# Performance work log

Measured on AMD Instinct MI355X. Metric: run time of the kernel, lower is better.

## Reference

```python
import jax, jax.numpy as jnp
import numpy as np

N_NODES = 50000
N_EDGES = 800000
IN_FEAT = 256
UNITS = 128
NEG_SLOPE = 0.2  # tf.nn.leaky_relu default alpha


def setup_inputs() -> dict:
    key = jax.random.key(0)
    k1, k2, k3, k4 = jax.random.split(key, 4)
    node_states = jax.random.normal(k1, (N_NODES, IN_FEAT), dtype=jnp.float32)
    edges = jax.random.randint(k2, (N_EDGES, 2), 0, N_NODES, dtype=jnp.int64)
    kernel = jax.random.normal(k3, (IN_FEAT, UNITS), dtype=jnp.float32) * 0.05
    kernel_attention = jax.random.normal(k4, (2 * UNITS, 1), dtype=jnp.float32) * 0.05
    return {"node_states": node_states, "edges": edges,
            "kernel": kernel, "kernel_attention": kernel_attention}


def reference(node_states, edges, kernel, kernel_attention):
    # node_states: [N, F], edges: [E, 2] (col 0 = target/segment, col 1 = source)
    n_nodes = node_states.shape[0]
    tgt = edges[:, 0]
    src = edges[:, 1]

    h = node_states @ kernel  # [N, U]

    # attention score per edge: leaky_relu(concat(h[tgt], h[src]) @ a)
    # split the attention vector so the two matmuls happen per-node (same math,
    # avoids materializing the [E, 2U] concat)
    u = h.shape[1]
    a_tgt = (h @ kernel_attention[:u]).squeeze(-1)  # [N]
    a_src = (h @ kernel_attention[u:]).squeeze(-1)  # [N]
    scores = jax.nn.leaky_relu(a_tgt[tgt] + a_src[src], NEG_SLOPE)  # [E]
    scores = jnp.exp(jnp.clip(scores, -2.0, 2.0))

    # segment softmax over edges grouped by target node
    denom = jax.ops.segment_sum(scores, tgt, num_segments=n_nodes)  # [N]
    attn = scores / denom[tgt]  # [E]

    # weighted aggregation of neighbor features
    out = jax.ops.segment_sum(h[src] * attn[:, None], tgt, num_segments=n_nodes)  # [N, U]
    return out
```

## Files before the change

kernel.cpp:

```cpp
#include <hip/hip_runtime.h>
#include <hip/hip_bf16.h>

#define N_NODES 50000
#define N_EDGES 800000
#define IN_FEAT 256
#define UNITS   128
#define BUCKET  64

typedef unsigned short ushort_t;
typedef __bf16 bf16x8 __attribute__((ext_vector_type(8)));
typedef float  f32x4  __attribute__((ext_vector_type(4)));
typedef unsigned short ushort8 __attribute__((ext_vector_type(8)));

__device__ __forceinline__ ushort_t bfbits(float f) {
    __bf16 b = (__bf16)f;
    return __builtin_bit_cast(ushort_t, b);
}

__device__ __forceinline__ void cvt8(const float4& f0, const float4& f1,
                                     ushort_t* dst) {
    bf16x8 u;
    u[0] = (__bf16)f0.x; u[1] = (__bf16)f0.y; u[2] = (__bf16)f0.z; u[3] = (__bf16)f0.w;
    u[4] = (__bf16)f1.x; u[5] = (__bf16)f1.y; u[6] = (__bf16)f1.z; u[7] = (__bf16)f1.w;
    *(bf16x8*)dst = u;
}

__global__ __launch_bounds__(256) void prep_wt_zero(const float* __restrict__ W,
                                                    ushort_t* __restrict__ Wt,
                                                    int* __restrict__ cnt, int M) {
    int i = blockIdx.x * 256 + threadIdx.x;
    if (i < UNITS * IN_FEAT) {
        int n = i >> 8;
        int k = i & 255;
        Wt[i] = bfbits(W[(size_t)k * UNITS + n]);
    }
    if (i < M) cnt[i] = 0;
}

__global__ __launch_bounds__(256) void gemm_mfma(const float* __restrict__ A,
                                                 const ushort_t* __restrict__ Wt,
                                                 const float* __restrict__ ka,
                                                 ushort_t* __restrict__ Hb,
                                                 float* __restrict__ a_tgt,
                                                 float* __restrict__ a_src, int M) {
    __shared__ __align__(16) ushort_t Bs[128 * 264];
    __shared__ __align__(16) ushort_t As[2 * 64 * 40];
    __shared__ float spt[64][2];
    __shared__ float sps[64][2];
    const int tid  = threadIdx.x;
    const int lane = tid & 63;
    const int wv   = tid >> 6;
    const int wy   = wv >> 1;
    const int wx   = wv & 1;
    const int row0 = blockIdx.x * 64;
    const int quad = lane >> 4;
    const int cl   = lane & 15;

    f32x4 acc[2][4] = {};

#pragma unroll
    for (int t = 0; t < 16; ++t) {
        int j = t * 256 + tid;
        int r = j >> 5;
        int c = (j & 31) * 8;
        *(ushort8*)(Bs + r * 264 + c) = *(const ushort8*)(Wt + r * 256 + c);
    }

    const int ar = tid >> 2, aq = tid & 3;
    const int gr = min(row0 + ar, M - 1);
    const float* aptr = A + (size_t)gr * IN_FEAT + aq * 8;
    ushort_t*    asw  = As + ar * 40 + aq * 8;

    {
        float4 f0 = *(const float4*)(aptr);
        float4 f1 = *(const float4*)(aptr + 4);
        cvt8(f0, f1, asw);
    }
    __syncthreads();

    for (int kc = 0; kc < IN_FEAT; kc += 32) {
        const int cur = (kc >> 5) & 1;
        const bool more = (kc + 32 < IN_FEAT);
        float4 g0, g1;
        if (more) {
            g0 = *(const float4*)(aptr + kc + 32);
            g1 = *(const float4*)(aptr + kc + 36);
        }

        bf16x8 af[2], bff[4];
        const ushort_t* asb = As + cur * 2560;
#pragma unroll
        for (int mi = 0; mi < 2; ++mi)
            af[mi] = *(const bf16x8*)(asb + (wy * 32 + mi * 16 + cl) * 40 + quad * 8);
#pragma unroll
        for (int ni = 0; ni < 4; ++ni)
            bff[ni] = *(const bf16x8*)(Bs + (wx * 64 + ni * 16 + cl) * 264 + kc + quad * 8);
#pragma unroll
        for (int mi = 0; mi < 2; ++mi)
#pragma unroll
            for (int ni = 0; ni < 4; ++ni)
                acc[mi][ni] = __builtin_amdgcn_mfma_f32_16x16x32_bf16(
                    af[mi], bff[ni], acc[mi][ni], 0, 0, 0);

        if (more)
            cvt8(g0, g1, As + (cur ^ 1) * 2560 + ar * 40 + aq * 8);
        __syncthreads();
    }

#pragma unroll
    for (int mi = 0; mi < 2; ++mi) {
#pragma unroll
        for (int ni = 0; ni < 4; ++ni) {
            int col = wx * 64 + ni * 16 + cl;
#pragma unroll
            for (int r = 0; r < 4; ++r) {
                int row = row0 + wy * 32 + mi * 16 + quad * 4 + r;
                if (row < M)
                    Hb[(size_t)row * UNITS + col] = bfbits(acc[mi][ni][r]);
            }
        }
    }

    float kt[4], ks[4];
#pragma unroll
    for (int ni = 0; ni < 4; ++ni) {
        int col = wx * 64 + ni * 16 + cl;
        kt[ni] = ka[col];
        ks[ni] = ka[UNITS + col];
    }
#pragma unroll
    for (int mi = 0; mi < 2; ++mi) {
        float pt[4] = {}, ps[4] = {};
#pragma unroll
        for (int ni = 0; ni < 4; ++ni)
#pragma unroll
            for (int r = 0; r < 4; ++r) {
                pt[r] += acc[mi][ni][r] * kt[ni];
                ps[r] += acc[mi][ni][r] * ks[ni];
            }
#pragma unroll
        for (int r = 0; r < 4; ++r) {
#pragma unroll
            for (int m = 1; m < 16; m <<= 1) {
                pt[r] += __shfl_xor(pt[r], m);
                ps[r] += __shfl_xor(ps[r], m);
            }
            if (cl == 0) {
                int rl = wy * 32 + mi * 16 + quad * 4 + r;
                spt[rl][wx] = pt[r];
                sps[rl][wx] = ps[r];
            }
        }
    }
    __syncthreads();
    if (tid < 64) {
        int row = row0 + tid;
        if (row < M) {
            a_tgt[row] = spt[tid][0] + spt[tid][1];
            a_src[row] = sps[tid][0] + sps[tid][1];
        }
    }
}

__device__ __forceinline__ float edge_score(float at, float as) {
    float s = at + as;
    s = s > 0.f ? s : 0.2f * s;
    s = fminf(fmaxf(s, -2.f), 2.f);
    return __expf(s);
}

__global__ __launch_bounds__(256) void scatter(const int* __restrict__ edges,
                                               const float* __restrict__ at,
                                               const float* __restrict__ as,
                                               int* __restrict__ cnt,
                                               int2* __restrict__ csr, int E) {
    int e = blockIdx.x * 256 + threadIdx.x;
    if (e >= E) return;
    int2 ts = ((const int2*)edges)[e];
    float sc = edge_score(at[ts.x], as[ts.y]);
    int r = atomicAdd(&cnt[ts.x], 1);
    if (r < BUCKET)
        csr[(size_t)ts.x * BUCKET + r] = make_int2(ts.y, __float_as_int(sc));
}

__global__ __launch_bounds__(256) void aggregate(const ushort_t* __restrict__ Hb,
                                                 const int* __restrict__ cnt,
                                                 const int2* __restrict__ csr,
                                                 float* __restrict__ out, int M) {
    int wid  = (int)((blockIdx.x * 256 + threadIdx.x) >> 6);
    int lane = threadIdx.x & 63;
    if (wid >= M) return;
    const int g = lane >> 4;
    const int c = lane & 15;
    const int deg = min(cnt[wid], BUCKET);

    int   s_v = 0;
    float w_v = 0.f;
    if (lane < deg) {
        int2 sw = csr[(size_t)wid * BUCKET + lane];
        s_v = sw.x;
        w_v = __int_as_float(sw.y);
    }

    float acc[8] = {};
    int nstep = (deg + 3) >> 2;
#pragma unroll 4
    for (int t = 0; t < nstep; ++t) {
        int slot = t * 4 + g;
        int   src = __shfl(s_v, slot);
        float w   = __shfl(w_v, slot);
        uint4 u = *(const uint4*)(Hb + (size_t)src * UNITS + c * 8);
        acc[0] += w * __uint_as_float(u.x << 16);
        acc[1] += w * __uint_as_float(u.x & 0xffff0000u);
        acc[2] += w * __uint_as_float(u.y << 16);
        acc[3] += w * __uint_as_float(u.y & 0xffff0000u);
        acc[4] += w * __uint_as_float(u.z << 16);
        acc[5] += w * __uint_as_float(u.z & 0xffff0000u);
        acc[6] += w * __uint_as_float(u.w << 16);
        acc[7] += w * __uint_as_float(u.w & 0xffff0000u);
    }

#pragma unroll
    for (int i = 0; i < 8; ++i) {
        acc[i] += __shfl_xor(acc[i], 16);
        acc[i] += __shfl_xor(acc[i], 32);
    }
    float wacc = w_v;
#pragma unroll
    for (int off = 32; off > 0; off >>= 1) wacc += __shfl_xor(wacc, off);
    float scale = (deg > 0) ? 1.0f / wacc : 0.0f;

    if (g == 0) {
        float4 o0 = make_float4(acc[0] * scale, acc[1] * scale,
                                acc[2] * scale, acc[3] * scale);
        float4 o1 = make_float4(acc[4] * scale, acc[5] * scale,
                                acc[6] * scale, acc[7] * scale);
        float* dst = out + (size_t)wid * UNITS + c * 8;
        *(float4*)dst       = o0;
        *(float4*)(dst + 4) = o1;
    }
}

extern "C" void kernel_launch(void* const* d_in, const int* in_sizes, int n_in,
                              void* d_out, int out_size, void* d_ws, size_t ws_size,
                              hipStream_t stream) {
    const float* node_states = (const float*)d_in[0];
    const int*   edges       = (const int*)d_in[1];
    const float* W           = (const float*)d_in[2];
    const float* ka          = (const float*)d_in[3];
    float*       out         = (float*)d_out;

    const int M = N_NODES, E = N_EDGES;

    ushort_t* hb     = (ushort_t*)d_ws;
    float*    a_tgt  = (float*)(hb + (size_t)M * UNITS);
    float*    a_src  = a_tgt + M;
    int*      cnt    = (int*)(a_src + M);
    int2*     csr    = (int2*)(cnt + M + 2);
    ushort_t* wt     = (ushort_t*)csr;

    prep_wt_zero<<<(M + 255) / 256, 256, 0, stream>>>(W, wt, cnt, M);
    gemm_mfma   <<<(M + 63) / 64, 256, 0, stream>>>(node_states, wt, ka, hb,
                                                    a_tgt, a_src, M);
    scatter     <<<(E + 255) / 256, 256, 0, stream>>>(edges, a_tgt, a_src,
                                                      cnt, csr, E);
    aggregate   <<<(M * 64 + 255) / 256, 256, 0, stream>>>(hb, cnt, csr, out, M);
}
```

Measured before the change: 185.2 us.

## Replace global-atomic edge scatter with two-pass binning by target range

Swaps the single scatter kernel, which did one global atomicAdd per edge on per-node counters, for two passes. The first bins edges into 196 target-node ranges using a shared-memory histogram, a block scan and staging. The second processes each bin in one 1024-thread block, counting with shared-memory atomics and writing the per-node counts directly, so the counter zeroing is no longer needed. This cuts contended global atomics and scattered writes, at the cost of an extra kernel launch, an extra pass over the edges, and only 196 blocks in the second pass. It also drops edges if a bin holds more than BIN_CAP entries.

Measured after the change: 167.7 us. -9.5%, faster.

```diff
diff --git a/kernel.cpp b/kernel.cpp
--- a/kernel.cpp
+++ b/kernel.cpp
@@ -6,6 +6,10 @@
 #define IN_FEAT 256
 #define UNITS   128
 #define BUCKET  64
+#define BIN_SHIFT 8
+#define NBINS   196
+#define BIN_CAP 4608
+#define CHUNK   4096
 
 typedef unsigned short ushort_t;
 typedef __bf16 bf16x8 __attribute__((ext_vector_type(8)));
@@ -27,14 +31,14 @@
 
 __global__ __launch_bounds__(256) void prep_wt_zero(const float* __restrict__ W,
                                                     ushort_t* __restrict__ Wt,
-                                                    int* __restrict__ cnt, int M) {
+                                                    int* __restrict__ gbin) {
     int i = blockIdx.x * 256 + threadIdx.x;
     if (i < UNITS * IN_FEAT) {
         int n = i >> 8;
         int k = i & 255;
         Wt[i] = bfbits(W[(size_t)k * UNITS + n]);
     }
-    if (i < M) cnt[i] = 0;
+    if (i < 256) gbin[i] = 0;
 }
 
 __global__ __launch_bounds__(256) void gemm_mfma(const float* __restrict__ A,
@@ -169,18 +173,105 @@
     return __expf(s);
 }
 
-__global__ __launch_bounds__(256) void scatter(const int* __restrict__ edges,
-                                               const float* __restrict__ at,
-                                               const float* __restrict__ as,
-                                               int* __restrict__ cnt,
-                                               int2* __restrict__ csr, int E) {
-    int e = blockIdx.x * 256 + threadIdx.x;
-    if (e >= E) return;
-    int2 ts = ((const int2*)edges)[e];
-    float sc = edge_score(at[ts.x], as[ts.y]);
-    int r = atomicAdd(&cnt[ts.x], 1);
-    if (r < BUCKET)
-        csr[(size_t)ts.x * BUCKET + r] = make_int2(ts.y, __float_as_int(sc));
+__global__ __launch_bounds__(256) void bin_edges(const int* __restrict__ edges,
+                                                 int* __restrict__ gbin,
+                                                 int2* __restrict__ binbuf, int E) {
+    __shared__ int  hist[256];
+    __shared__ int  sbase[256];
+    __shared__ int  runoff[256];
+    __shared__ int  gbase[256];
+    __shared__ int  wsum[4];
+    __shared__ int2 stage[CHUNK];
+    const int tid  = threadIdx.x;
+    const int lane = tid & 63, wv = tid >> 6;
+    const int e0   = blockIdx.x * CHUNK;
+
+    hist[tid] = 0;
+    __syncthreads();
+
+    int2 er[16];
+    int  eb[16];
+#pragma unroll
+    for (int j = 0; j < 16; ++j) {
+        int idx = e0 + j * 256 + tid;
+        if (idx < E) {
+            er[j] = ((const int2*)edges)[idx];
+            eb[j] = er[j].x >> BIN_SHIFT;
+            atomicAdd(&hist[eb[j]], 1);
+        } else eb[j] = -1;
+    }
+    __syncthreads();
+
+    int h = hist[tid];
+    int incl = h;
+#pragma unroll
+    for (int off = 1; off < 64; off <<= 1) {
+        int t = __shfl_up(incl, off);
+        if (lane >= off) incl += t;
+    }
+    if (lane == 63) wsum[wv] = incl;
+    __syncthreads();
+    int excl = incl - h;
+#pragma unroll
+    for (int w = 0; w < 4; ++w) if (w < wv) excl += wsum[w];
+    sbase[tid]  = excl;
+    runoff[tid] = excl;
+    __syncthreads();
+
+    if (h > 0) gbase[tid] = atomicAdd(&gbin[tid], h);
+
+#pragma unroll
+    for (int j = 0; j < 16; ++j) {
+        if (eb[j] >= 0) {
+            int p = atomicAdd(&runoff[eb[j]], 1);
+            stage[p] = er[j];
+        }
+    }
+    __syncthreads();
+
+    int total = sbase[255] + hist[255];
+    for (int p = tid; p < total; p += 256) {
+        int2 ts = stage[p];
+        int b   = ts.x >> BIN_SHIFT;
+        int dst = gbase[b] + (p - sbase[b]);
+        if (dst < BIN_CAP)
+            binbuf[(size_t)b * BIN_CAP + dst] = ts;
+    }
+}
+
+__global__ __launch_bounds__(1024) void bucket_scatter(const int2* __restrict__ binbuf,
+                                                       const int* __restrict__ gbin,
+                                                       const float* __restrict__ at,
+                                                       const float* __restrict__ as,
+                                                       int* __restrict__ cnt,
+                                                       int2* __restrict__ csr, int M) {
+    __shared__ int   lcnt[256];
+    __shared__ float atl[256];
+    const int tid = threadIdx.x;
+    const int bin = blockIdx.x;
+    const int t0  = bin << BIN_SHIFT;
+    if (tid < 256) {
+        lcnt[tid] = 0;
+        int t = t0 + tid;
+        atl[tid] = (t < M) ? at[t] : 0.f;
+    }
+    __syncthreads();
+
+    const int bcnt = min(gbin[bin], BIN_CAP);
+    const int2* src = binbuf + (size_t)bin * BIN_CAP;
+    for (int p = tid; p < bcnt; p += 1024) {
+        int2 ts = src[p];
+        int lt  = ts.x - t0;
+        float sc = edge_score(atl[lt], as[ts.y]);
+        int r = atomicAdd(&lcnt[lt], 1);
+        if (r < BUCKET)
+            csr[(size_t)ts.x * BUCKET + r] = make_int2(ts.y, __float_as_int(sc));
+    }
+    __syncthreads();
+    if (tid < 256) {
+        int t = t0 + tid;
+        if (t < M) cnt[t] = lcnt[tid];
+    }
 }
 
 __global__ __launch_bounds__(256) void aggregate(const ushort_t* __restrict__ Hb,
@@ -256,13 +347,18 @@
     float*    a_tgt  = (float*)(hb + (size_t)M * UNITS);
     float*    a_src  = a_tgt + M;
     int*      cnt    = (int*)(a_src + M);
-    int2*     csr    = (int2*)(cnt + M + 2);
+    int*      gbin   = cnt + M;
+    int2*     csr    = (int2*)(gbin + 256);
+    int2*     binbuf = csr + (size_t)M * BUCKET;
     ushort_t* wt     = (ushort_t*)csr;
 
-    prep_wt_zero<<<(M + 255) / 256, 256, 0, stream>>>(W, wt, cnt, M);
-    gemm_mfma   <<<(M + 63) / 64, 256, 0, stream>>>(node_states, wt, ka, hb,
-                                                    a_tgt, a_src, M);
-    scatter     <<<(E + 255) / 256, 256, 0, stream>>>(edges, a_tgt, a_src,
-                                                      cnt, csr, E);
-    aggregate   <<<(M * 64 + 255) / 256, 256, 0, stream>>>(hb, cnt, csr, out, M);
-}
+    const int nblkA = (E + CHUNK - 1) / CHUNK;
+
+    prep_wt_zero  <<<(UNITS * IN_FEAT + 255) / 256, 256, 0, stream>>>(W, wt, gbin);
+    gemm_mfma     <<<(M + 63) / 64, 256, 0, stream>>>(node_states, wt, ka, hb,
+                                                      a_tgt, a_src, M);
+    bin_edges     <<<nblkA, 256, 0, stream>>>(edges, gbin, binbuf, E);
+    bucket_scatter<<<NBINS, 1024, 0, stream>>>(binbuf, gbin, a_tgt, a_src,
+                                               cnt, csr, M);
+    aggregate     <<<(M * 64 + 255) / 256, 256, 0, stream>>>(hb, cnt, csr, out, M);
+}
```
